# Kernel tuning notes

Measured on AMD Instinct MI355X. Metric: run time of the kernel, lower is better.

The kernel has to match this reference:

```python
import jax, jax.numpy as jnp
import numpy as np

EPS = 1e-5  # torch LayerNorm default


def _channel_ln(h, g, b):
    # h: (B, C, N); LayerNorm over channel dim C (biased variance)
    m = jnp.mean(h, axis=1, keepdims=True)
    v = jnp.mean((h - m) ** 2, axis=1, keepdims=True)
    return (h - m) * jax.lax.rsqrt(v + EPS) * g[None, :, None] + b[None, :, None]


def setup_inputs() -> dict:
    key = jax.random.key(0)
    ks = jax.random.split(key, 16)
    B, Cin, Cout, N = 8, 64, 128, 4096
    w = lambda i, shape: jax.random.normal(ks[i], shape, jnp.float32) * 0.02
    return {
        "x": jax.random.normal(ks[0], (B, Cin, N), jnp.float32),
        "p": jax.random.normal(ks[1], (B, 3, N), jnp.float32),
        "W_in": w(2, (Cout, Cin)), "b_in": jnp.zeros((Cout,), jnp.float32),
        "W_q": w(3, (Cout, Cout)),
        "W_k": w(4, (Cout, Cout)),
        "W_v": w(5, (Cout, Cout)),
        "W_d1": w(6, (Cout, 3)), "b_d1": jnp.zeros((Cout,), jnp.float32),
        "W_d2": w(7, (Cout, Cout)), "b_d2": jnp.zeros((Cout,), jnp.float32),
        "W_a": w(8, (Cout, Cout)), "b_a": jnp.zeros((Cout,), jnp.float32),
        "g1": jnp.ones((Cout,), jnp.float32), "be1": jnp.zeros((Cout,), jnp.float32),
        "g2": jnp.ones((Cout,), jnp.float32), "be2": jnp.zeros((Cout,), jnp.float32),
        "W_f1": w(9, (4 * Cout, Cout)), "b_f1": jnp.zeros((4 * Cout,), jnp.float32),
        "W_f2": w(10, (Cout, 4 * Cout)), "b_f2": jnp.zeros((Cout,), jnp.float32),
        "knn_k": 16,
    }


def reference(x, p, W_in, b_in, W_q, W_k, W_v, W_d1, b_d1, W_d2, b_d2,
              W_a, b_a, g1, be1, g2, be2, W_f1, b_f1, W_f2, b_f2, knn_k):
    h = jnp.einsum('oc,bcn->bon', W_in, x) + b_in[None, :, None]  # (B,C,N)
    B, C, N = h.shape
    k = min(int(knn_k), max(1, N - 1))

    h_n = _channel_ln(h, g1, be1)

    # knn on coordinates p: negative squared distance, self excluded
    pt = jnp.swapaxes(p, 1, 2)                                    # (B,N,3)
    xx = jnp.sum(pt * pt, axis=-1)                                # (B,N)
    dist = 2.0 * jnp.einsum('bnd,bmd->bnm', pt, pt) - xx[:, :, None] - xx[:, None, :]
    dist = dist - 1e9 * jnp.eye(N, dtype=dist.dtype)[None]
    idx = jax.lax.top_k(dist, k)[1]                               # (B,N,k) int32

    hn_t = jnp.swapaxes(h_n, 1, 2)                                # (B,N,C)
    q_all = hn_t @ W_q.T
    k_all = hn_t @ W_k.T
    v_all = hn_t @ W_v.T

    bi = jnp.arange(B)[:, None, None]
    k_j = k_all[bi, idx]                                          # (B,N,k,C)
    v_j = v_all[bi, idx]                                          # (B,N,k,C)
    p_j = pt[bi, idx]                                             # (B,N,k,3)

    rel = pt[:, :, None, :] - p_j                                 # (B,N,k,3)
    d = jax.nn.relu(rel @ W_d1.T + b_d1) @ W_d2.T + b_d2          # (B,N,k,C)

    logits = (q_all[:, :, None, :] - k_j + d) @ W_a.T + b_a       # (B,N,k,C)
    a = jax.nn.softmax(logits, axis=2)                            # softmax over k neighbors
    y = jnp.sum(a * (v_j + d), axis=2)                            # (B,N,C)

    h = h + jnp.swapaxes(y, 1, 2)
    h2t = jnp.swapaxes(_channel_ln(h, g2, be2), 1, 2)             # (B,N,C)
    f = jax.nn.relu(h2t @ W_f1.T + b_f1) @ W_f2.T + b_f2          # (B,N,C)
    return h + jnp.swapaxes(f, 1, 2)                              # (B,C,N)
```

## Files before the change

### kernel.cpp

```cpp
#include <hip/hip_runtime.h>
#include <stdint.h>


typedef __attribute__((ext_vector_type(8))) short s8;
typedef __attribute__((ext_vector_type(4))) float f4;

#define MFMA16(a,b,c) __builtin_amdgcn_mfma_f32_16x16x32_bf16(a,b,c,0,0,0)

__device__ __forceinline__ float bf2f(unsigned short u){
  unsigned x = ((unsigned)u) << 16; return __builtin_bit_cast(float, x);
}
__device__ __forceinline__ unsigned short f2bf(float f){
  unsigned x = __builtin_bit_cast(unsigned, f);
  x = x + 0x7FFFu + ((x >> 16) & 1u);
  return (unsigned short)(x >> 16);
}

__device__ __forceinline__ void ce32(unsigned &a, unsigned &b){
  unsigned mn = min(a, b), mx = max(a, b);
  a = mn; b = mx;
}
__device__ __forceinline__ void sort16_u32(unsigned v[16]){
  #pragma unroll
  for (int p = 1; p < 16; p <<= 1){
    #pragma unroll
    for (int k = p; k >= 1; k >>= 1){
      #pragma unroll
      for (int j = k % p; j + k < 16; j += 2*k){
        #pragma unroll
        for (int i = 0; i < k; ++i){
          if (i + j + k < 16){
            if (((i+j) / (2*p)) == ((i+j+k) / (2*p))) ce32(v[i+j], v[i+j+k]);
          }
        }
      }
    }
  }
}
__device__ __forceinline__ void bitonic16_u32(unsigned v[16]){
  #pragma unroll
  for (int k = 8; k >= 1; k >>= 1){
    #pragma unroll
    for (int i = 0; i < 16; ++i){
      if ((i & k) == 0) ce32(v[i], v[i | k]);
    }
  }
}
__device__ __forceinline__ void merge16r(unsigned top[16], const unsigned w[16],
                                         unsigned &r17){
  unsigned t[16], m17 = 0xFFFFFFFFu;
  #pragma unroll
  for (int i = 0; i < 16; ++i){
    unsigned a = top[i], b = w[15 - i];
    t[i] = min(a, b);
    m17 = min(m17, max(a, b));
  }
  bitonic16_u32(t);
  #pragma unroll
  for (int i = 0; i < 16; ++i) top[i] = t[i];
  r17 = min(r17, m17);
}
__device__ __forceinline__ void drainP(unsigned* br, int &cnt, unsigned top[16],
                                       unsigned &r17, unsigned &thr){
  unsigned v[16];
  #pragma unroll
  for (int j = 0; j < 16; ++j){
    unsigned t = br[j];
    v[j] = (j < cnt) ? t : 0xFFFFFFFFu;
  }
  cnt = 0;
  sort16_u32(v);
  merge16r(top, v, r17);
  thr = top[15];
}

__global__ __launch_bounds__(128) void k_p1(const float* __restrict__ W_a,
    const float* __restrict__ W_k, const float* __restrict__ W_q, const float* __restrict__ W_d2,
    float* __restrict__ tk, float* __restrict__ tq, float* __restrict__ td){
  int which = blockIdx.x >> 7, row = blockIdx.x & 127, c = threadIdx.x;
  const float* X = (which == 0) ? W_k : ((which == 1) ? W_q : W_d2);
  float* O = (which == 0) ? tk : ((which == 1) ? tq : td);
  float acc = 0.f;
  #pragma unroll 8
  for (int i = 0; i < 128; ++i) acc += W_a[row*128 + i] * X[i*128 + c];
  O[row*128 + c] = acc;
}

__global__ __launch_bounds__(256) void k_pack(
    const float* __restrict__ p, const float* __restrict__ W_v,
    const float* __restrict__ W_d1, const float* __restrict__ b_d1,
    const float* __restrict__ W_in, const float* __restrict__ W_f1, const float* __restrict__ W_f2,
    const float* __restrict__ W_a, const float* __restrict__ b_a, const float* __restrict__ b_d2,
    const float* __restrict__ W_d2,
    const float* __restrict__ tk, const float* __restrict__ tq, const float* __restrict__ td,
    float4* __restrict__ pp, unsigned short* __restrict__ wcatf, unsigned short* __restrict__ wf1f,
    unsigned short* __restrict__ wf2f, unsigned short* __restrict__ wd2f,
    unsigned short* __restrict__ wdaf, unsigned short* __restrict__ w1f,
    unsigned short* __restrict__ winf, float* __restrict__ ball){
  int id0 = blockIdx.x * blockDim.x + threadIdx.x;
  int stride = gridDim.x * blockDim.x;
  for (int i = id0; i < 32768; i += stride){
    int b = i >> 12, m = i & 4095;
    float xx = p[(b*3 + 0)*4096 + m];
    float yy = p[(b*3 + 1)*4096 + m];
    float zz = p[(b*3 + 2)*4096 + m];
    pp[i] = float4{xx, yy, zz, xx*xx + yy*yy + zz*zz};
  }
  for (int i = id0; i < 49152; i += stride){
    int tg = i >> 11, s = (i >> 9) & 3, l = (i >> 3) & 63, j = i & 7;
    int row = tg*16 + (l & 15), k = s*32 + (l >> 4)*8 + j;
    float v;
    if (row < 128) v = tk[row*128 + k];
    else if (row < 256) v = W_v[(row - 128)*128 + k];
    else v = tq[(row - 256)*128 + k];
    wcatf[i] = f2bf(v);
  }
  for (int i = id0; i < 65536; i += stride){
    int tg = i >> 11, s = (i >> 9) & 3, l = (i >> 3) & 63, j = i & 7;
    int row = tg*16 + (l & 15), k = s*32 + (l >> 4)*8 + j;
    wf1f[i] = f2bf(W_f1[row*128 + k]);
  }
  for (int i = id0; i < 65536; i += stride){
    int mt = i >> 13, s = (i >> 9) & 15, l = (i >> 3) & 63, j = i & 7;
    int row = mt*16 + (l & 15), k = s*32 + (l >> 4)*8 + j;
    wf2f[i] = f2bf(W_f2[row*512 + k]);
  }
  for (int i = id0; i < 16384; i += stride){
    int tg = i >> 11, s = (i >> 9) & 3, l = (i >> 3) & 63, j = i & 7;
    int row = tg*16 + (l & 15), k = s*32 + (l >> 4)*8 + j;
    wd2f[i] = f2bf(W_d2[row*128 + k]);
  }
  for (int i = id0; i < 16384; i += stride){
    int tg = i >> 11, s = (i >> 9) & 3, l = (i >> 3) & 63, j = i & 7;
    int row = tg*16 + (l & 15), k = s*32 + (l >> 4)*8 + j;
    wdaf[i] = f2bf(td[row*128 + k]);
  }
  for (int i = id0; i < 4096; i += stride){
    int tg = i >> 9, l = (i >> 3) & 63, j = i & 7;
    int c = tg*16 + (l & 15);
    float v = 0.f;
    if (l < 16 && j < 4) v = (j < 3) ? W_d1[c*3 + j] : b_d1[c];
    w1f[i] = f2bf(v);
  }
  for (int i = id0; i < 8192; i += stride){
    int tg = i >> 10, s = (i >> 9) & 1, l = (i >> 3) & 63, j = i & 7;
    int row = tg*16 + (l & 15), k = s*32 + (l >> 4)*8 + j;
    winf[i] = f2bf(W_in[row*64 + k]);
  }
  for (int o = id0; o < 128; o += stride){
    float acc = b_a[o];
    for (int c = 0; c < 128; ++c) acc += W_a[o*128 + c] * b_d2[c];
    ball[o] = acc;
  }
}

__global__ __launch_bounds__(256) void k_a(const float* __restrict__ x,
    const unsigned short* __restrict__ WINF, const float* __restrict__ b_in,
    const float* __restrict__ g1, const float* __restrict__ be1,
    float* __restrict__ H, unsigned short* __restrict__ HN){
  __shared__ unsigned short xT[64][72];
  int tid = threadIdx.x;
  int bb = blockIdx.x >> 6;
  int n0 = (blockIdx.x & 63) * 64;
  for (int i = tid; i < 4096; i += 256){
    int c = i >> 6, nn = i & 63;
    xT[nn][c] = f2bf(x[((size_t)(bb*64 + c))*4096 + n0 + nn]);
  }
  __syncthreads();
  int lane = tid & 63, w = tid >> 6, m16 = lane & 15, g = lane >> 4;
  const char* xb = (const char*)&xT[0][0];
  s8 a0 = *(const s8*)(xb + (w*16 + m16)*144 + 16*g);
  s8 a1 = *(const s8*)(xb + (w*16 + m16)*144 + 64 + 16*g);
  const f4 zf = {0.f, 0.f, 0.f, 0.f};
  f4 acc[8];
  #pragma unroll
  for (int t = 0; t < 8; ++t) acc[t] = zf;
  #pragma unroll
  for (int t = 0; t < 8; ++t){
    s8 b0 = *(const s8*)(WINF + ((size_t)(t*2 + 0)*64 + lane)*8);
    s8 b1 = *(const s8*)(WINF + ((size_t)(t*2 + 1)*64 + lane)*8);
    acc[t] = MFMA16(a0, b0, acc[t]);
    acc[t] = MFMA16(a1, b1, acc[t]);
  }
  float mean[4], rstd[4];
  #pragma unroll
  for (int r = 0; r < 4; ++r){
    float ls = 0.f, lq = 0.f;
    #pragma unroll
    for (int t = 0; t < 8; ++t){
      float v = acc[t][r] + b_in[t*16 + m16];
      ls += v; lq += v*v;
    }
    ls += __shfl_xor(ls, 1); ls += __shfl_xor(ls, 2); ls += __shfl_xor(ls, 4); ls += __shfl_xor(ls, 8);
    lq += __shfl_xor(lq, 1); lq += __shfl_xor(lq, 2); lq += __shfl_xor(lq, 4); lq += __shfl_xor(lq, 8);
    float mn = ls * (1.f/128.f);
    float vr = lq * (1.f/128.f) - mn*mn;
    mean[r] = mn;
    rstd[r] = rsqrtf(vr + 1e-5f);
  }
  int ptbase = blockIdx.x*64 + w*16;
  #pragma unroll
  for (int t = 0; t < 8; ++t){
    int o = t*16 + m16;
    float bi = b_in[o], gg = g1[o], be = be1[o];
    #pragma unroll
    for (int r = 0; r < 4; ++r){
      int pt = ptbase + 4*g + r;
      float v = acc[t][r] + bi;
      H[(size_t)pt*128 + o] = v;
      HN[(size_t)pt*128 + o] = f2bf((v - mean[r])*rstd[r]*gg + be);
    }
  }
}

template<int MODE>
__global__ __launch_bounds__(256) void k_gemm(const unsigned short* __restrict__ A,
    const unsigned short* __restrict__ Btab, const float* __restrict__ bias,
    unsigned short* __restrict__ out){
  int lane = threadIdx.x & 63, w = threadIdx.x >> 6;
  int m0 = blockIdx.x*64 + w*16;
  int by = blockIdx.y;
  int m16 = lane & 15, g = lane >> 4;
  const f4 zf = {0.f, 0.f, 0.f, 0.f};
  f4 acc[8];
  #pragma unroll
  for (int t = 0; t < 8; ++t) acc[t] = zf;
  #pragma unroll
  for (int s = 0; s < 4; ++s){
    s8 af = *(const s8*)(A + ((size_t)(m0 + m16))*128 + s*32 + g*8);
    #pragma unroll
    for (int t = 0; t < 8; ++t){
      s8 bf = *(const s8*)(Btab + ((size_t)((by*8 + t)*4 + s)*64 + lane)*8);
      acc[t] = MFMA16(af, bf, acc[t]);
    }
  }
  #pragma unroll
  for (int t = 0; t < 8; ++t){
    int col = by*128 + t*16 + m16;
    #pragma unroll
    for (int r = 0; r < 4; ++r){
      int pt = m0 + 4*g + r;
      float v = acc[t][r];
      if (MODE == 0){
        int pos = (col < 128) ? 2*col : ((col < 256) ? 2*(col - 128) + 1 : col);
        out[(size_t)pt*384 + pos] = f2bf(v);
      } else {
        v = fmaxf(v + bias[col], 0.f);
        out[(size_t)pt*512 + col] = f2bf(v);
      }
    }
  }
}

__global__ __launch_bounds__(256) void k_f2(const unsigned short* __restrict__ wf2f,
    const unsigned short* __restrict__ Z, const float* __restrict__ b_f2,
    float* __restrict__ out){
  int lane = threadIdx.x & 63, w = threadIdx.x >> 6;
  int mt = blockIdx.x*4 + w;
  int p0 = blockIdx.y*128;
  int m16 = lane & 15, g = lane >> 4;
  const f4 zf = {0.f, 0.f, 0.f, 0.f};
  f4 acc[8];
  #pragma unroll
  for (int t = 0; t < 8; ++t) acc[t] = zf;
  #pragma unroll 4
  for (int s = 0; s < 16; ++s){
    s8 af = *(const s8*)(wf2f + ((size_t)(mt*16 + s)*64 + lane)*8);
    #pragma unroll
    for (int t = 0; t < 8; ++t){
      s8 bf = *(const s8*)(Z + (size_t)(p0 + t*16 + m16)*512 + s*32 + g*8);
      acc[t] = MFMA16(af, bf, acc[t]);
    }
  }
  #pragma unroll
  for (int t = 0; t < 8; ++t){
    #pragma unroll
    for (int r = 0; r < 4; ++r){
      int o = mt*16 + 4*g + r;
      int pt = p0 + t*16 + m16;
      int b = pt >> 12, n = pt & 4095;
      size_t ix = (((size_t)(b*128 + o)) << 12) | (unsigned)n;
      out[ix] += acc[t][r] + b_f2[o];
    }
  }
}

__global__ __launch_bounds__(256, 8) void k_knn(const float4* __restrict__ PP,
    int* __restrict__ IDXo){
  __shared__ __align__(16) char smem[17920];
  int tid = threadIdx.x;
  int b = blockIdx.x >> 7;
  int tile = blockIdx.x & 127;
  int q = tid & 31;
  int sub = tid >> 5;
  int qn = tile*32 + q;
  const float4* pb = PP + (size_t)b*4096;
  float4 me = pb[qn];
  int base = sub << 9;

  unsigned* br32 = (unsigned*)(smem + tid*68);

  unsigned top32[16];
  #pragma unroll
  for (int j = 0; j < 16; ++j) top32[j] = 0xFFFFFFFFu;
  unsigned r17 = 0xFFFFFFFFu;
  unsigned thr = 0xFFFFFFFFu;
  int cnt = 0;
  float4 c0 = pb[base+0], c1 = pb[base+1], c2 = pb[base+2], c3 = pb[base+3];
  #pragma unroll 1
  for (int ii = 0; ii < 128; ++ii){
    float4 d0 = c0, d1 = c1, d2v = c2, d3 = c3;
    int nb = base + (((ii + 1) & 127) << 2);
    c0 = pb[nb+0]; c1 = pb[nb+1]; c2 = pb[nb+2]; c3 = pb[nb+3];
    int m0 = base + ii*4;
    {
      float dx = me.x-d0.x, dy = me.y-d0.y, dz = me.z-d0.z;
      unsigned key = (__builtin_bit_cast(unsigned, dx*dx+dy*dy+dz*dz) & 0xFFFFF000u) | (unsigned)m0;
      if (m0 != qn){ if (key < thr){ br32[cnt] = key; ++cnt; } else r17 = min(r17, key); }
    }
    {
      float dx = me.x-d1.x, dy = me.y-d1.y, dz = me.z-d1.z;
      unsigned key = (__builtin_bit_cast(unsigned, dx*dx+dy*dy+dz*dz) & 0xFFFFF000u) | (unsigned)(m0+1);
      if (m0+1 != qn){ if (key < thr){ br32[cnt] = key; ++cnt; } else r17 = min(r17, key); }
    }
    {
      float dx = me.x-d2v.x, dy = me.y-d2v.y, dz = me.z-d2v.z;
      unsigned key = (__builtin_bit_cast(unsigned, dx*dx+dy*dy+dz*dz) & 0xFFFFF000u) | (unsigned)(m0+2);
      if (m0+2 != qn){ if (key < thr){ br32[cnt] = key; ++cnt; } else r17 = min(r17, key); }
    }
    {
      float dx = me.x-d3.x, dy = me.y-d3.y, dz = me.z-d3.z;
      unsigned key = (__builtin_bit_cast(unsigned, dx*dx+dy*dy+dz*dz) & 0xFFFFF000u) | (unsigned)(m0+3);
      if (m0+3 != qn){ if (key < thr){ br32[cnt] = key; ++cnt; } else r17 = min(r17, key); }
    }
    if (__any(cnt >= 13)) drainP(br32, cnt, top32, r17, thr);
  }
  drainP(br32, cnt, top32, r17, thr);

  unsigned* pub = (unsigned*)smem;
  #pragma unroll
  for (int step = 4; step >= 1; step >>= 1){
    __syncthreads();
    if (sub >= step && sub < 2*step){
      unsigned* row = pub + (size_t)((sub - step)*32 + q)*17;
      #pragma unroll
      for (int j = 0; j < 16; ++j) row[j] = top32[j];
      row[16] = r17;
    }
    __syncthreads();
    if (sub < step){
      unsigned other[16];
      unsigned* row = pub + (size_t)(sub*32 + q)*17;
      #pragma unroll
      for (int j = 0; j < 16; ++j) other[j] = row[j];
      r17 = min(r17, row[16]);
      merge16r(top32, other, r17);
    }
  }

  unsigned key16 = top32[15];
  bool flag = false;
  if (sub == 0){
    flag = ((r17 >> 12) - (key16 >> 12)) <= 1u;
    if (!flag){
      int* op = IDXo + ((size_t)(b*4096 + qn))*16;
      #pragma unroll
      for (int j = 0; j < 16; ++j) op[j] = (int)(top32[j] & 0xFFFu);
    }
  }

  if ((tid >> 6) == 0){
    int lane = tid & 63;
    unsigned long long flags = __ballot(flag);
    int* pcnt = (int*)(smem + 17408);
    unsigned* pool = (unsigned*)(smem + 17412);
    while (flags){
      int L = __ffsll((long long)flags) - 1;
      flags &= flags - 1;
      int qf = tile*32 + L;
      float qx = __shfl(me.x, L), qy = __shfl(me.y, L), qz = __shfl(me.z, L);
      unsigned k16 = __shfl(key16, L);
      unsigned t16 = k16 >> 12;
      unsigned bhi = (t16 >= 0xFFFFDu) ? 0xFFFFFFFFu : ((t16 + 2) << 12);
      if (lane == 0) atomicExch(pcnt, 0);
      #pragma unroll 4
      for (int it = 0; it < 64; ++it){
        int m = it*64 + lane;
        float4 cd = pb[m];
        float dx = qx-cd.x, dy = qy-cd.y, dz = qz-cd.z;
        unsigned bits = __builtin_bit_cast(unsigned, dx*dx+dy*dy+dz*dz);
        if (m != qf && bits < bhi){
          int s = atomicAdd(pcnt, 1);
          if (s < 64) pool[s] = (unsigned)m;
        }
      }
      int pn = atomicAdd(pcnt, 0);
      if (pn > 64) pn = 64;
      unsigned long long kk = ~0ull;
      if (lane < pn){
        int m = pool[lane];
        float4 cd = pb[m];
        double ddx = (double)qx - (double)cd.x;
        double ddy = (double)qy - (double)cd.y;
        double ddz = (double)qz - (double)cd.z;
        double d2 = ddx*ddx + ddy*ddy + ddz*ddz;
        kk = (__builtin_bit_cast(unsigned long long, d2) & ~0xFFFull) | (unsigned)m;
      }
      #pragma unroll
      for (int k2 = 2; k2 <= 64; k2 <<= 1){
        #pragma unroll
        for (int j = k2 >> 1; j >= 1; j >>= 1){
          unsigned long long o = __shfl_xor(kk, j);
          bool up = ((lane & k2) == 0);
          bool keepmin = (((lane & j) == 0) == up);
          unsigned long long mn = kk < o ? kk : o;
          unsigned long long mx = kk < o ? o : kk;
          kk = keepmin ? mn : mx;
        }
      }
      if (lane < 16)
        IDXo[((size_t)(b*4096 + qf))*16 + lane] = (int)(unsigned)(kk & 0xFFFull);
    }
  }
}

__global__ __launch_bounds__(256) void k_attn(const float* __restrict__ pcoord,
    const int* __restrict__ IDX, const unsigned short* __restrict__ QKV,
    const unsigned short* __restrict__ W1F, const unsigned short* __restrict__ WD2F,
    const unsigned short* __restrict__ WDAF, const float* __restrict__ b_d2,
    const float* __restrict__ BALL, unsigned short* __restrict__ Y){
  __shared__ __align__(16) char smem[18432];
  __shared__ int idx_sh[4][2][16];
  int tid = threadIdx.x;
  int w = tid >> 6, lane = tid & 63;
  int m16 = lane & 15, g = lane >> 4;
  int P0 = blockIdx.x*8 + w*2;
  char* wbase = smem + w*4608;
  const f4 zf = {0.f, 0.f, 0.f, 0.f};
  if (lane < 16){
    #pragma unroll
    for (int q = 0; q < 2; ++q) idx_sh[w][q][lane] = IDX[(size_t)(P0 + q)*16 + lane];
  }
  unsigned short* t1s = (unsigned short*)wbase;
  s8 a[2][4];
  #pragma unroll
  for (int q = 0; q < 2; ++q){
    int pt = P0 + q;
    int bq = pt >> 12, nn = pt & 4095;
    const float* pb = pcoord + (size_t)bq*3*4096;
    s8 arel = {0,0,0,0,0,0,0,0};
    if (lane < 16){
      int jn = idx_sh[w][q][m16];
      float rx = pb[nn] - pb[jn];
      float ry = pb[4096 + nn] - pb[4096 + jn];
      float rz = pb[8192 + nn] - pb[8192 + jn];
      arel[0] = (short)f2bf(rx); arel[1] = (short)f2bf(ry);
      arel[2] = (short)f2bf(rz); arel[3] = (short)0x3F80;
    }
    f4 t1a[8];
    #pragma unroll
    for (int t = 0; t < 8; ++t){
      s8 bw = *(const s8*)(W1F + ((size_t)t*64 + lane)*8);
      t1a[t] = MFMA16(arel, bw, zf);
    }
    #pragma unroll
    for (int t = 0; t < 8; ++t){
      int c = t*16 + m16;
      #pragma unroll
      for (int r = 0; r < 4; ++r){
        int m = 4*g + r;
        int byt = (m*256 + c*2) ^ ((m & 7) << 4);
        t1s[byt >> 1] = f2bf(fmaxf(t1a[t][r], 0.f));
      }
    }
    const char* t1b = (const char*)t1s;
    #pragma unroll
    for (int s = 0; s < 4; ++s){
      int byt = (m16*256 + 64*s + 16*g) ^ ((m16 & 7) << 4);
      a[q][s] = *(const s8*)(t1b + byt);
    }
  }
  #pragma unroll 1
  for (int pass = 0; pass < 4; ++pass){
    asm volatile("s_waitcnt lgkmcnt(0)" ::: "memory");
    __builtin_amdgcn_sched_barrier(0);
    uint4 gk[2][2];
    float qv[2];
    #pragma unroll
    for (int q = 0; q < 2; ++q){
      int pt = P0 + q, bq = pt >> 12;
      #pragma unroll
      for (int i2 = 0; i2 < 2; ++i2){
        int mm = i2*8 + (lane >> 3);
        int jn = idx_sh[w][q][mm];
        gk[q][i2] = *(const uint4*)((const char*)QKV
            + ((size_t)(bq*4096 + jn))*768 + pass*128 + (lane & 7)*16);
      }
      qv[q] = bf2f(QKV[(size_t)pt*384 + 256 + pass*32 + (lane & 31)]);
    }
    #pragma unroll
    for (int q = 0; q < 2; ++q){
      #pragma unroll
      for (int i2 = 0; i2 < 2; ++i2)
        *(uint4*)(wbase + q*2304 + (i2*8 + (lane >> 3))*144 + (lane & 7)*16) = gk[q][i2];
    }
    #pragma unroll
    for (int tl = 0; tl < 2; ++tl){
      int tg = pass*2 + tl;
      f4 dacc[2], lacc[2];
      #pragma unroll
      for (int q = 0; q < 2; ++q){ dacc[q] = zf; lacc[q] = zf; }
      #pragma unroll
      for (int s = 0; s < 4; ++s){
        s8 wd2 = *(const s8*)(WD2F + ((size_t)(tg*4 + s)*64 + lane)*8);
        s8 wda = *(const s8*)(WDAF + ((size_t)(tg*4 + s)*64 + lane)*8);
        #pragma unroll
        for (int q = 0; q < 2; ++q){
          dacc[q] = MFMA16(a[q][s], wd2, dacc[q]);
          lacc[q] = MFMA16(a[q][s], wda, lacc[q]);
        }
      }
      int col = tg*16 + m16;
      float bd2c = b_d2[col];
      float ballc = BALL[col];
      #pragma unroll
      for (int q = 0; q < 2; ++q){
        int pt = P0 + q;
        float qbase = __shfl(qv[q], tl*16 + m16) + ballc;
        float lg[4], dd[4], vv[4];
        #pragma unroll
        for (int r = 0; r < 4; ++r){
          int m = 4*g + r;
          unsigned kvp = *(const unsigned*)(wbase + q*2304 + m*144 + (tl*16 + m16)*4);
          float ka = bf2f((unsigned short)(kvp & 0xFFFFu));
          vv[r] = bf2f((unsigned short)(kvp >> 16));
          lg[r] = lacc[q][r] + qbase - ka;
          dd[r] = dacc[q][r] + bd2c;
        }
        float e0 = __expf(lg[0]), e1 = __expf(lg[1]);
        float e2 = __expf(lg[2]), e3 = __expf(lg[3]);
        float ss = e0 + e1 + e2 + e3;
        ss += __shfl_xor(ss, 16); ss += __shfl_xor(ss, 32);
        float inv = 1.f / ss;
        float yp = e0*(vv[0] + dd[0]) + e1*(vv[1] + dd[1])
                 + e2*(vv[2] + dd[2]) + e3*(vv[3] + dd[3]);
        yp *= inv;
        yp += __shfl_xor(yp, 16); yp += __shfl_xor(yp, 32);
        if (lane < 16) Y[(size_t)pt*128 + col] = f2bf(yp);
      }
    }
  }
}

__global__ __launch_bounds__(256) void k_d1(const float* __restrict__ H,
    const unsigned short* __restrict__ Y, const float* __restrict__ g2,
    const float* __restrict__ be2, float* __restrict__ outp,
    unsigned short* __restrict__ HN2){
  __shared__ float tile[128*65];
  int tid = threadIdx.x;
  int w = tid >> 6, lane = tid & 63;
  int pt16 = lane & 15, g = lane >> 4;
  int n64 = w*16 + pt16;
  int ptbase = blockIdx.x * 64;
  int pt = ptbase + n64;
  int c0 = g*32;
  const float4* h4 = (const float4*)(H + (size_t)pt*128 + c0);
  const uint4*  y4 = (const uint4*)((const char*)Y + (size_t)pt*256 + (size_t)c0*2);
  float h2[32];
  float ls = 0.f, lq = 0.f;
  #pragma unroll
  for (int i = 0; i < 4; ++i){
    float4 ha = h4[2*i], hb = h4[2*i + 1];
    uint4 yv = y4[i];
    float v0 = ha.x + bf2f((unsigned short)(yv.x & 0xFFFFu));
    float v1 = ha.y + bf2f((unsigned short)(yv.x >> 16));
    float v2 = ha.z + bf2f((unsigned short)(yv.y & 0xFFFFu));
    float v3 = ha.w + bf2f((unsigned short)(yv.y >> 16));
    float v4 = hb.x + bf2f((unsigned short)(yv.z & 0xFFFFu));
    float v5 = hb.y + bf2f((unsigned short)(yv.z >> 16));
    float v6 = hb.z + bf2f((unsigned short)(yv.w & 0xFFFFu));
    float v7 = hb.w + bf2f((unsigned short)(yv.w >> 16));
    h2[8*i+0]=v0; h2[8*i+1]=v1; h2[8*i+2]=v2; h2[8*i+3]=v3;
    h2[8*i+4]=v4; h2[8*i+5]=v5; h2[8*i+6]=v6; h2[8*i+7]=v7;
    ls += v0+v1+v2+v3+v4+v5+v6+v7;
    lq += v0*v0+v1*v1+v2*v2+v3*v3+v4*v4+v5*v5+v6*v6+v7*v7;
  }
  ls += __shfl_xor(ls, 16); ls += __shfl_xor(ls, 32);
  lq += __shfl_xor(lq, 16); lq += __shfl_xor(lq, 32);
  float mn = ls * (1.f/128.f);
  float vr = lq * (1.f/128.f) - mn*mn;
  float rs = rsqrtf(vr + 1e-5f);
  const float4* g4  = (const float4*)(g2 + c0);
  const float4* be4 = (const float4*)(be2 + c0);
  #pragma unroll
  for (int i = 0; i < 4; ++i){
    float4 ga = g4[2*i], gb = g4[2*i+1], ba = be4[2*i], bb2 = be4[2*i+1];
    unsigned uu[4];
    uu[0] = (unsigned)f2bf((h2[8*i+0]-mn)*rs*ga.x + ba.x)
          | ((unsigned)f2bf((h2[8*i+1]-mn)*rs*ga.y + ba.y) << 16);
    uu[1] = (unsigned)f2bf((h2[8*i+2]-mn)*rs*ga.z + ba.z)
          | ((unsigned)f2bf((h2[8*i+3]-mn)*rs*ga.w + ba.w) << 16);
    uu[2] = (unsigned)f2bf((h2[8*i+4]-mn)*rs*gb.x + bb2.x)
          | ((unsigned)f2bf((h2[8*i+5]-mn)*rs*gb.y + bb2.y) << 16);
    uu[3] = (unsigned)f2bf((h2[8*i+6]-mn)*rs*gb.z + bb2.z)
          | ((unsigned)f2bf((h2[8*i+7]-mn)*rs*gb.w + bb2.w) << 16);
    *(uint4*)((char*)HN2 + (size_t)pt*256 + (size_t)c0*2 + i*16)
        = make_uint4(uu[0], uu[1], uu[2], uu[3]);
  }
  int swz = g << 4;
  #pragma unroll
  for (int k = 0; k < 32; ++k)
    tile[(c0 + k)*65 + (n64 ^ swz)] = h2[k];
  __syncthreads();
  int bb = ptbase >> 12;
  int nb = ptbase & 4095;
  #pragma unroll 8
  for (int k = 0; k < 32; ++k){
    int c = w*32 + k;
    float v = tile[c*65 + (lane ^ ((((unsigned)c >> 5) & 3) << 4))];
    outp[(((size_t)(bb*128 + c)) << 12) | (unsigned)(nb + lane)] = v;
  }
}

extern "C" void kernel_launch(void* const* d_in, const int* in_sizes, int n_in,
                              void* d_out, int out_size, void* d_ws, size_t ws_size,
                              hipStream_t stream){
  const float* x    = (const float*)d_in[0];
  const float* p    = (const float*)d_in[1];
  const float* W_in = (const float*)d_in[2];
  const float* b_in = (const float*)d_in[3];
  const float* W_q  = (const float*)d_in[4];
  const float* W_k  = (const float*)d_in[5];
  const float* W_v  = (const float*)d_in[6];
  const float* W_d1 = (const float*)d_in[7];
  const float* b_d1 = (const float*)d_in[8];
  const float* W_d2 = (const float*)d_in[9];
  const float* b_d2 = (const float*)d_in[10];
  const float* W_a  = (const float*)d_in[11];
  const float* b_a  = (const float*)d_in[12];
  const float* g1   = (const float*)d_in[13];
  const float* be1  = (const float*)d_in[14];
  const float* g2   = (const float*)d_in[15];
  const float* be2  = (const float*)d_in[16];
  const float* W_f1 = (const float*)d_in[17];
  const float* b_f1 = (const float*)d_in[18];
  const float* W_f2 = (const float*)d_in[19];
  const float* b_f2 = (const float*)d_in[20];
  float* out = (float*)d_out;
  char* ws = (char*)d_ws;

  float*          H    = (float*)(ws + 0);
  unsigned short* HN   = (unsigned short*)(ws + 16777216);
  unsigned short* QKV  = (unsigned short*)(ws + 25165824);
  unsigned short* Z    = (unsigned short*)(ws + 16777216);
  unsigned short* Y    = (unsigned short*)(ws + 50331648);
  unsigned short* HN2  = (unsigned short*)(ws + 58720256);
  int*            IDX  = (int*)(ws + 67108864);
  float4*         PP   = (float4*)(ws + 69206016);
  char* tab = ws + 69730304;
  unsigned short* WCATF = (unsigned short*)(tab + 0);
  unsigned short* WF1F  = (unsigned short*)(tab + 98304);
  unsigned short* WF2F  = (unsigned short*)(tab + 229376);
  unsigned short* WD2F  = (unsigned short*)(tab + 360448);
  unsigned short* WDAF  = (unsigned short*)(tab + 393216);
  unsigned short* W1F   = (unsigned short*)(tab + 425984);
  unsigned short* WINF  = (unsigned short*)(tab + 434176);
  float*          BALL  = (float*)(tab + 450560);
  float*          TK    = (float*)(tab + 451072);
  float*          TQ    = (float*)(tab + 516608);
  float*          TD    = (float*)(tab + 582144);

  k_p1<<<dim3(384), dim3(128), 0, stream>>>(W_a, W_k, W_q, W_d2, TK, TQ, TD);
  k_pack<<<dim3(256), dim3(256), 0, stream>>>(p, W_v, W_d1, b_d1, W_in, W_f1, W_f2,
      W_a, b_a, b_d2, W_d2, TK, TQ, TD,
      PP, WCATF, WF1F, WF2F, WD2F, WDAF, W1F, WINF, BALL);
  k_knn<<<dim3(1024), dim3(256), 0, stream>>>(PP, IDX);
  k_a<<<dim3(512), dim3(256), 0, stream>>>(x, WINF, b_in, g1, be1, H, HN);
  k_gemm<0><<<dim3(512, 3), dim3(256), 0, stream>>>(HN, WCATF, nullptr, QKV);
  k_attn<<<dim3(4096), dim3(256), 0, stream>>>(p, IDX, QKV, W1F, WD2F, WDAF, b_d2, BALL, Y);
  k_d1<<<dim3(512), dim3(256), 0, stream>>>(H, Y, g2, be2, out, HN2);
  k_gemm<1><<<dim3(512, 4), dim3(256), 0, stream>>>(HN2, WF1F, b_f1, Z);
  k_f2<<<dim3(2, 256), dim3(256), 0, stream>>>(WF2F, Z, b_f2, out);
}
```

Before: 332.5 us.

## Seed kNN threshold with sorted prefix and split candidates across more sub-groups

The kNN kernel now handles 16 queries per block with 16 sub-groups, each scanning 256 candidates, so the grid doubles. Each thread first sorts and merges its initial 64 candidates with a sorting network to set a tight top-16 threshold before the streaming scan. The goal is fewer buffer drains and better load balance. The cost is a deeper shared-memory merge tree, with four levels and more syncs, plus extra register pressure from the unrolled seeding.

```diff
diff --git a/kernel.cpp b/kernel.cpp
--- a/kernel.cpp
+++ b/kernel.cpp
@@ -289,60 +289,66 @@
     int* __restrict__ IDXo){
   __shared__ __align__(16) char smem[17920];
   int tid = threadIdx.x;
-  int b = blockIdx.x >> 7;
-  int tile = blockIdx.x & 127;
-  int q = tid & 31;
-  int sub = tid >> 5;
-  int qn = tile*32 + q;
+  int b = blockIdx.x >> 8;
+  int tile = blockIdx.x & 255;
+  int q = tid & 15;
+  int sub = tid >> 4;
+  int qn = tile*16 + q;
   const float4* pb = PP + (size_t)b*4096;
   float4 me = pb[qn];
-  int base = sub << 9;
-
+  const float4* cb = pb + (sub << 8);
+
+  unsigned top32[16];
+  unsigned r17 = 0xFFFFFFFFu;
+  #pragma unroll
+  for (int c = 0; c < 4; ++c){
+    unsigned v[16];
+    #pragma unroll
+    for (int j = 0; j < 16; ++j){
+      float4 cd = cb[c*16 + j];
+      int m = (sub << 8) + c*16 + j;
+      float dx = me.x-cd.x, dy = me.y-cd.y, dz = me.z-cd.z;
+      unsigned key = (__builtin_bit_cast(unsigned, dx*dx+dy*dy+dz*dz) & 0xFFFFF000u) | (unsigned)m;
+      v[j] = (m == qn) ? 0xFFFFFFFFu : key;
+    }
+    sort16_u32(v);
+    if (c == 0){
+      #pragma unroll
+      for (int j = 0; j < 16; ++j) top32[j] = v[j];
+    } else {
+      merge16r(top32, v, r17);
+    }
+  }
+  unsigned thr = top32[15];
+
+  int cnt = 0;
   unsigned* br32 = (unsigned*)(smem + tid*68);
-
-  unsigned top32[16];
-  #pragma unroll
-  for (int j = 0; j < 16; ++j) top32[j] = 0xFFFFFFFFu;
-  unsigned r17 = 0xFFFFFFFFu;
-  unsigned thr = 0xFFFFFFFFu;
-  int cnt = 0;
-  float4 c0 = pb[base+0], c1 = pb[base+1], c2 = pb[base+2], c3 = pb[base+3];
   #pragma unroll 1
-  for (int ii = 0; ii < 128; ++ii){
-    float4 d0 = c0, d1 = c1, d2v = c2, d3 = c3;
-    int nb = base + (((ii + 1) & 127) << 2);
-    c0 = pb[nb+0]; c1 = pb[nb+1]; c2 = pb[nb+2]; c3 = pb[nb+3];
-    int m0 = base + ii*4;
-    {
-      float dx = me.x-d0.x, dy = me.y-d0.y, dz = me.z-d0.z;
-      unsigned key = (__builtin_bit_cast(unsigned, dx*dx+dy*dy+dz*dz) & 0xFFFFF000u) | (unsigned)m0;
-      if (m0 != qn){ if (key < thr){ br32[cnt] = key; ++cnt; } else r17 = min(r17, key); }
-    }
-    {
-      float dx = me.x-d1.x, dy = me.y-d1.y, dz = me.z-d1.z;
-      unsigned key = (__builtin_bit_cast(unsigned, dx*dx+dy*dy+dz*dz) & 0xFFFFF000u) | (unsigned)(m0+1);
-      if (m0+1 != qn){ if (key < thr){ br32[cnt] = key; ++cnt; } else r17 = min(r17, key); }
-    }
-    {
-      float dx = me.x-d2v.x, dy = me.y-d2v.y, dz = me.z-d2v.z;
-      unsigned key = (__builtin_bit_cast(unsigned, dx*dx+dy*dy+dz*dz) & 0xFFFFF000u) | (unsigned)(m0+2);
-      if (m0+2 != qn){ if (key < thr){ br32[cnt] = key; ++cnt; } else r17 = min(r17, key); }
-    }
-    {
-      float dx = me.x-d3.x, dy = me.y-d3.y, dz = me.z-d3.z;
-      unsigned key = (__builtin_bit_cast(unsigned, dx*dx+dy*dy+dz*dz) & 0xFFFFF000u) | (unsigned)(m0+3);
-      if (m0+3 != qn){ if (key < thr){ br32[cnt] = key; ++cnt; } else r17 = min(r17, key); }
-    }
-    if (__any(cnt >= 13)) drainP(br32, cnt, top32, r17, thr);
+  for (int oo = 0; oo < 12; ++oo){
+    const float4* ob = cb + 64 + oo*16;
+    int mb = (sub << 8) + 64 + oo*16;
+    #pragma unroll
+    for (int jg = 0; jg < 4; ++jg){
+      #pragma unroll
+      for (int u = 0; u < 4; ++u){
+        int j = jg*4 + u;
+        float4 cd = ob[j];
+        int m = mb + j;
+        float dx = me.x-cd.x, dy = me.y-cd.y, dz = me.z-cd.z;
+        unsigned key = (__builtin_bit_cast(unsigned, dx*dx+dy*dy+dz*dz) & 0xFFFFF000u) | (unsigned)m;
+        if (m != qn){ if (key < thr){ br32[cnt] = key; ++cnt; } else r17 = min(r17, key); }
+      }
+      if (__any(cnt >= 13)) drainP(br32, cnt, top32, r17, thr);
+    }
   }
   drainP(br32, cnt, top32, r17, thr);
 
   unsigned* pub = (unsigned*)smem;
   #pragma unroll
-  for (int step = 4; step >= 1; step >>= 1){
+  for (int step = 8; step >= 1; step >>= 1){
     __syncthreads();
     if (sub >= step && sub < 2*step){
-      unsigned* row = pub + (size_t)((sub - step)*32 + q)*17;
+      unsigned* row = pub + (size_t)((sub - step)*16 + q)*17;
       #pragma unroll
       for (int j = 0; j < 16; ++j) row[j] = top32[j];
       row[16] = r17;
@@ -350,7 +356,7 @@
     __syncthreads();
     if (sub < step){
       unsigned other[16];
-      unsigned* row = pub + (size_t)(sub*32 + q)*17;
+      unsigned* row = pub + (size_t)(sub*16 + q)*17;
       #pragma unroll
       for (int j = 0; j < 16; ++j) other[j] = row[j];
       r17 = min(r17, row[16]);
@@ -377,7 +383,7 @@
     while (flags){
       int L = __ffsll((long long)flags) - 1;
       flags &= flags - 1;
-      int qf = tile*32 + L;
+      int qf = tile*16 + L;
       float qx = __shfl(me.x, L), qy = __shfl(me.y, L), qz = __shfl(me.z, L);
       unsigned k16 = __shfl(key16, L);
       unsigned t16 = k16 >> 12;
@@ -674,7 +680,7 @@
   k_pack<<<dim3(256), dim3(256), 0, stream>>>(p, W_v, W_d1, b_d1, W_in, W_f1, W_f2,
       W_a, b_a, b_d2, W_d2, TK, TQ, TD,
       PP, WCATF, WF1F, WF2F, WD2F, WDAF, W1F, WINF, BALL);
-  k_knn<<<dim3(1024), dim3(256), 0, stream>>>(PP, IDX);
+  k_knn<<<dim3(2048), dim3(256), 0, stream>>>(PP, IDX);
   k_a<<<dim3(512), dim3(256), 0, stream>>>(x, WINF, b_in, g1, be1, H, HN);
   k_gemm<0><<<dim3(512, 3), dim3(256), 0, stream>>>(HN, WCATF, nullptr, QKV);
   k_attn<<<dim3(4096), dim3(256), 0, stream>>>(p, IDX, QKV, W1F, WD2F, WDAF, b_d2, BALL, Y);
```

New measurement: 369.1 us. +11.0%, slower.

## Replace brute-force kNN with uniform-grid spatial hashing and ring search

Applied to the files above, without the earlier changes.

Points are binned into a 32^3 uniform grid per batch, built with atomic counting, a prefix scan and a scatter into cell-sorted order. Each query wave then scans expanding rings of cells, keeping per-lane top-16 lists that are merged across the wave with shuffles, and stops once the ring boundary distance exceeds the current 17th-best distance. This removes the all-pairs distance evaluation of the old kernel. It adds a memset and three extra small kernels. Performance depends on the point distribution matching the assumed [-5,5] grid extent, although clamping keeps results correct for any input.

```diff
diff --git a/kernel.cpp b/kernel.cpp
--- a/kernel.cpp
+++ b/kernel.cpp
@@ -20,23 +20,6 @@
   unsigned mn = min(a, b), mx = max(a, b);
   a = mn; b = mx;
 }
-__device__ __forceinline__ void sort16_u32(unsigned v[16]){
-  #pragma unroll
-  for (int p = 1; p < 16; p <<= 1){
-    #pragma unroll
-    for (int k = p; k >= 1; k >>= 1){
-      #pragma unroll
-      for (int j = k % p; j + k < 16; j += 2*k){
-        #pragma unroll
-        for (int i = 0; i < k; ++i){
-          if (i + j + k < 16){
-            if (((i+j) / (2*p)) == ((i+j+k) / (2*p))) ce32(v[i+j], v[i+j+k]);
-          }
-        }
-      }
-    }
-  }
-}
 __device__ __forceinline__ void bitonic16_u32(unsigned v[16]){
   #pragma unroll
   for (int k = 8; k >= 1; k >>= 1){
@@ -60,18 +43,39 @@
   for (int i = 0; i < 16; ++i) top[i] = t[i];
   r17 = min(r17, m17);
 }
-__device__ __forceinline__ void drainP(unsigned* br, int &cnt, unsigned top[16],
-                                       unsigned &r17, unsigned &thr){
-  unsigned v[16];
-  #pragma unroll
-  for (int j = 0; j < 16; ++j){
-    unsigned t = br[j];
-    v[j] = (j < cnt) ? t : 0xFFFFFFFFu;
-  }
-  cnt = 0;
-  sort16_u32(v);
-  merge16r(top, v, r17);
-  thr = top[15];
+__device__ __forceinline__ void insert16(unsigned top16[16], unsigned &r17, unsigned key){
+  if (key < top16[15]){
+    unsigned cur = key;
+    #pragma unroll
+    for (int i = 0; i < 16; ++i){
+      unsigned lo = min(cur, top16[i]);
+      unsigned hi = max(cur, top16[i]);
+      top16[i] = lo; cur = hi;
+    }
+    r17 = min(r17, cur);
+  } else {
+    r17 = min(r17, key);
+  }
+}
+__device__ __forceinline__ void wave_merge(const unsigned loc[16], unsigned lr17,
+                                           unsigned out[16], unsigned &or17){
+  #pragma unroll
+  for (int j = 0; j < 16; ++j) out[j] = loc[j];
+  unsigned rr = lr17;
+  #pragma unroll
+  for (int s = 1; s < 64; s <<= 1){
+    unsigned oth[16];
+    #pragma unroll
+    for (int j = 0; j < 16; ++j) oth[j] = (unsigned)__shfl_xor((int)out[j], s);
+    unsigned ro = (unsigned)__shfl_xor((int)rr, s);
+    rr = min(rr, ro);
+    merge16r(out, oth, rr);
+  }
+  or17 = rr;
+}
+__device__ __forceinline__ int cell1(float x){
+  int c = (int)floorf((x + 5.f) * 3.2f);
+  return min(max(c, 0), 31);
 }
 
 __global__ __launch_bounds__(128) void k_p1(const float* __restrict__ W_a,
@@ -96,7 +100,8 @@
     float4* __restrict__ pp, unsigned short* __restrict__ wcatf, unsigned short* __restrict__ wf1f,
     unsigned short* __restrict__ wf2f, unsigned short* __restrict__ wd2f,
     unsigned short* __restrict__ wdaf, unsigned short* __restrict__ w1f,
-    unsigned short* __restrict__ winf, float* __restrict__ ball){
+    unsigned short* __restrict__ winf, float* __restrict__ ball,
+    unsigned* __restrict__ ccnt){
   int id0 = blockIdx.x * blockDim.x + threadIdx.x;
   int stride = gridDim.x * blockDim.x;
   for (int i = id0; i < 32768; i += stride){
@@ -105,6 +110,8 @@
     float yy = p[(b*3 + 1)*4096 + m];
     float zz = p[(b*3 + 2)*4096 + m];
     pp[i] = float4{xx, yy, zz, xx*xx + yy*yy + zz*zz};
+    int cid = (cell1(xx)*32 + cell1(yy))*32 + cell1(zz);
+    atomicAdd(&ccnt[b*32768 + cid], 1u);
   }
   for (int i = id0; i < 49152; i += stride){
     int tg = i >> 11, s = (i >> 9) & 3, l = (i >> 3) & 63, j = i & 7;
@@ -152,6 +159,174 @@
     for (int c = 0; c < 128; ++c) acc += W_a[o*128 + c] * b_d2[c];
     ball[o] = acc;
   }
+}
+
+__global__ __launch_bounds__(1024) void k_scan(unsigned* __restrict__ CNTCUR,
+    unsigned* __restrict__ OFF){
+  __shared__ unsigned ps[1024];
+  int b = blockIdx.x, t = threadIdx.x;
+  unsigned* cnt = CNTCUR + (size_t)b*32768;
+  int base = t*32;
+  unsigned run = 0;
+  #pragma unroll
+  for (int i = 0; i < 32; ++i) run += cnt[base + i];
+  ps[t] = run;
+  __syncthreads();
+  for (int st = 1; st < 1024; st <<= 1){
+    unsigned v = (t >= st) ? ps[t - st] : 0u;
+    __syncthreads();
+    ps[t] += v;
+    __syncthreads();
+  }
+  unsigned run2 = (t == 0) ? 0u : ps[t-1];
+  #pragma unroll
+  for (int i = 0; i < 32; ++i){
+    unsigned v = cnt[base + i];
+    OFF[(size_t)b*32769 + base + i] = run2;
+    cnt[base + i] = run2;
+    run2 += v;
+  }
+  if (t == 1023) OFF[(size_t)b*32769 + 32768] = 4096u;
+}
+
+__global__ __launch_bounds__(256) void k_scatter(const float4* __restrict__ PP,
+    unsigned* __restrict__ CUR, float4* __restrict__ SPTS){
+  int i = blockIdx.x*256 + threadIdx.x;
+  float4 pt = PP[i];
+  int b = i >> 12, n = i & 4095;
+  int cid = (cell1(pt.x)*32 + cell1(pt.y))*32 + cell1(pt.z);
+  unsigned pos = atomicAdd(&CUR[(size_t)b*32768 + cid], 1u);
+  SPTS[(size_t)b*4096 + pos] = float4{pt.x, pt.y, pt.z,
+                                      __builtin_bit_cast(float, n)};
+}
+
+__global__ __launch_bounds__(256) void k_knng(const float4* __restrict__ PP,
+    const float4* __restrict__ SPTS, const unsigned* __restrict__ OFF,
+    int* __restrict__ IDXo){
+  __shared__ unsigned pool_sh[4][64];
+  int wv = threadIdx.x >> 6;
+  int lane = threadIdx.x & 63;
+  int wid = blockIdx.x*4 + wv;
+  int b = wid >> 12, n = wid & 4095;
+  const float4 me = PP[(size_t)b*4096 + n];
+  const float4* sp = SPTS + (size_t)b*4096;
+  const unsigned* off = OFF + (size_t)b*32769;
+  float qx = me.x, qy = me.y, qz = me.z;
+  int cx = cell1(qx), cy = cell1(qy), cz = cell1(qz);
+
+  unsigned top16[16];
+  #pragma unroll
+  for (int j = 0; j < 16; ++j) top16[j] = 0xFFFFFFFFu;
+  unsigned r17 = 0xFFFFFFFFu;
+  unsigned tot = 0;
+  unsigned g16[16];
+  unsigned gr17 = 0xFFFFFFFFu;
+
+  auto do_range = [&](int cbase, int za, int zb){
+    unsigned s = off[cbase + za];
+    unsigned e = off[cbase + zb + 1];
+    int len = (int)(e - s);
+    int first = ((int)lane - (int)tot) & 63;
+    for (int i = first; i < len; i += 64){
+      float4 cd = sp[s + i];
+      int m = __builtin_bit_cast(int, cd.w);
+      float dx = qx - cd.x, dy = qy - cd.y, dz = qz - cd.z;
+      float d2 = dx*dx + dy*dy + dz*dz;
+      unsigned key = (__builtin_bit_cast(unsigned, d2) & 0xFFFFF000u) | (unsigned)m;
+      if (m != n) insert16(top16, r17, key);
+    }
+    tot += (unsigned)len;
+  };
+
+  bool done = false;
+  #pragma unroll 1
+  for (int R = 1; R <= 32 && !done; ++R){
+    int x0 = max(cx-R, 0), x1 = min(cx+R, 31);
+    int y0 = max(cy-R, 0), y1 = min(cy+R, 31);
+    #pragma unroll 1
+    for (int gx = x0; gx <= x1; ++gx){
+      int dxm = (gx > cx) ? (gx - cx) : (cx - gx);
+      #pragma unroll 1
+      for (int gy = y0; gy <= y1; ++gy){
+        int dym = (gy > cy) ? (gy - cy) : (cy - gy);
+        int dm = max(dxm, dym);
+        int cbase = (gx*32 + gy)*32;
+        if (R == 1 || dm == R){
+          do_range(cbase, max(cz-R, 0), min(cz+R, 31));
+        } else {
+          if (cz - R >= 0)  do_range(cbase, cz-R, cz-R);
+          if (cz + R <= 31) do_range(cbase, cz+R, cz+R);
+        }
+      }
+    }
+    wave_merge(top16, r17, g16, gr17);
+    float bd = 1e30f;
+    if (cx - R >= 0)  bd = fminf(bd, qx - (-5.f + (float)(cx-R)*0.3125f));
+    if (cx + R <= 31) bd = fminf(bd, (-5.f + (float)(cx+R+1)*0.3125f) - qx);
+    if (cy - R >= 0)  bd = fminf(bd, qy - (-5.f + (float)(cy-R)*0.3125f));
+    if (cy + R <= 31) bd = fminf(bd, (-5.f + (float)(cy+R+1)*0.3125f) - qy);
+    if (cz - R >= 0)  bd = fminf(bd, qz - (-5.f + (float)(cz-R)*0.3125f));
+    if (cz + R <= 31) bd = fminf(bd, (-5.f + (float)(cz+R+1)*0.3125f) - qz);
+    if (bd > 1e29f){
+      done = true;
+    } else if (gr17 != 0xFFFFFFFFu){
+      unsigned ub = (gr17 & 0xFFFFF000u) + 0x1000u;
+      float d2ub = __builtin_bit_cast(float, ub) * (1.f + 1e-5f);
+      float bl = bd * bd * (1.f - 1e-5f);
+      if (bl > d2ub) done = true;
+    }
+  }
+
+  unsigned key16 = g16[15];
+  bool flag = ((gr17 >> 12) - (key16 >> 12)) <= 1u;
+  if (!flag){
+    if (lane < 16) IDXo[(size_t)wid*16 + lane] = (int)(g16[lane] & 0xFFFu);
+    return;
+  }
+  unsigned t16 = key16 >> 12;
+  unsigned bhi = (t16 >= 0xFFFFDu) ? 0xFFFFFFFFu : ((t16 + 2) << 12);
+  unsigned pcnt = 0;
+  const float4* pb = PP + (size_t)b*4096;
+  #pragma unroll 4
+  for (int it = 0; it < 64; ++it){
+    int m = it*64 + lane;
+    float4 cd = pb[m];
+    float dx = qx-cd.x, dy = qy-cd.y, dz = qz-cd.z;
+    unsigned bits = __builtin_bit_cast(unsigned, dx*dx+dy*dy+dz*dz);
+    bool cond = (m != n) && (bits < bhi);
+    unsigned long long mk = __ballot(cond);
+    if (cond){
+      int pos = (int)pcnt + __popcll(mk & ((1ull << lane) - 1ull));
+      if (pos < 64) pool_sh[wv][pos] = (unsigned)m;
+    }
+    pcnt += (unsigned)__popcll(mk);
+  }
+  asm volatile("s_waitcnt lgkmcnt(0)" ::: "memory");
+  int pn = (int)min(pcnt, 64u);
+  unsigned long long kk = ~0ull;
+  if (lane < pn){
+    int m = (int)pool_sh[wv][lane];
+    float4 cd = pb[m];
+    double ddx = (double)qx - (double)cd.x;
+    double ddy = (double)qy - (double)cd.y;
+    double ddz = (double)qz - (double)cd.z;
+    double d2 = ddx*ddx + ddy*ddy + ddz*ddz;
+    kk = (__builtin_bit_cast(unsigned long long, d2) & ~0xFFFull) | (unsigned)m;
+  }
+  #pragma unroll
+  for (int k2 = 2; k2 <= 64; k2 <<= 1){
+    #pragma unroll
+    for (int j = k2 >> 1; j >= 1; j >>= 1){
+      unsigned long long o = __shfl_xor(kk, j);
+      bool up = ((lane & k2) == 0);
+      bool keepmin = (((lane & j) == 0) == up);
+      unsigned long long mn = kk < o ? kk : o;
+      unsigned long long mx = kk < o ? o : kk;
+      kk = keepmin ? mn : mx;
+    }
+  }
+  if (lane < 16)
+    IDXo[(size_t)wid*16 + lane] = (int)(unsigned)(kk & 0xFFFull);
 }
 
 __global__ __launch_bounds__(256) void k_a(const float* __restrict__ x,
@@ -281,145 +456,6 @@
       int b = pt >> 12, n = pt & 4095;
       size_t ix = (((size_t)(b*128 + o)) << 12) | (unsigned)n;
       out[ix] += acc[t][r] + b_f2[o];
-    }
-  }
-}
-
-__global__ __launch_bounds__(256, 8) void k_knn(const float4* __restrict__ PP,
-    int* __restrict__ IDXo){
-  __shared__ __align__(16) char smem[17920];
-  int tid = threadIdx.x;
-  int b = blockIdx.x >> 7;
-  int tile = blockIdx.x & 127;
-  int q = tid & 31;
-  int sub = tid >> 5;
-  int qn = tile*32 + q;
-  const float4* pb = PP + (size_t)b*4096;
-  float4 me = pb[qn];
-  int base = sub << 9;
-
-  unsigned* br32 = (unsigned*)(smem + tid*68);
-
-  unsigned top32[16];
-  #pragma unroll
-  for (int j = 0; j < 16; ++j) top32[j] = 0xFFFFFFFFu;
-  unsigned r17 = 0xFFFFFFFFu;
-  unsigned thr = 0xFFFFFFFFu;
-  int cnt = 0;
-  float4 c0 = pb[base+0], c1 = pb[base+1], c2 = pb[base+2], c3 = pb[base+3];
-  #pragma unroll 1
-  for (int ii = 0; ii < 128; ++ii){
-    float4 d0 = c0, d1 = c1, d2v = c2, d3 = c3;
-    int nb = base + (((ii + 1) & 127) << 2);
-    c0 = pb[nb+0]; c1 = pb[nb+1]; c2 = pb[nb+2]; c3 = pb[nb+3];
-    int m0 = base + ii*4;
-    {
-      float dx = me.x-d0.x, dy = me.y-d0.y, dz = me.z-d0.z;
-      unsigned key = (__builtin_bit_cast(unsigned, dx*dx+dy*dy+dz*dz) & 0xFFFFF000u) | (unsigned)m0;
-      if (m0 != qn){ if (key < thr){ br32[cnt] = key; ++cnt; } else r17 = min(r17, key); }
-    }
-    {
-      float dx = me.x-d1.x, dy = me.y-d1.y, dz = me.z-d1.z;
-      unsigned key = (__builtin_bit_cast(unsigned, dx*dx+dy*dy+dz*dz) & 0xFFFFF000u) | (unsigned)(m0+1);
-      if (m0+1 != qn){ if (key < thr){ br32[cnt] = key; ++cnt; } else r17 = min(r17, key); }
-    }
-    {
-      float dx = me.x-d2v.x, dy = me.y-d2v.y, dz = me.z-d2v.z;
-      unsigned key = (__builtin_bit_cast(unsigned, dx*dx+dy*dy+dz*dz) & 0xFFFFF000u) | (unsigned)(m0+2);
-      if (m0+2 != qn){ if (key < thr){ br32[cnt] = key; ++cnt; } else r17 = min(r17, key); }
-    }
-    {
-      float dx = me.x-d3.x, dy = me.y-d3.y, dz = me.z-d3.z;
-      unsigned key = (__builtin_bit_cast(unsigned, dx*dx+dy*dy+dz*dz) & 0xFFFFF000u) | (unsigned)(m0+3);
-      if (m0+3 != qn){ if (key < thr){ br32[cnt] = key; ++cnt; } else r17 = min(r17, key); }
-    }
-    if (__any(cnt >= 13)) drainP(br32, cnt, top32, r17, thr);
-  }
-  drainP(br32, cnt, top32, r17, thr);
-
-  unsigned* pub = (unsigned*)smem;
-  #pragma unroll
-  for (int step = 4; step >= 1; step >>= 1){
-    __syncthreads();
-    if (sub >= step && sub < 2*step){
-      unsigned* row = pub + (size_t)((sub - step)*32 + q)*17;
-      #pragma unroll
-      for (int j = 0; j < 16; ++j) row[j] = top32[j];
-      row[16] = r17;
-    }
-    __syncthreads();
-    if (sub < step){
-      unsigned other[16];
-      unsigned* row = pub + (size_t)(sub*32 + q)*17;
-      #pragma unroll
-      for (int j = 0; j < 16; ++j) other[j] = row[j];
-      r17 = min(r17, row[16]);
-      merge16r(top32, other, r17);
-    }
-  }
-
-  unsigned key16 = top32[15];
-  bool flag = false;
-  if (sub == 0){
-    flag = ((r17 >> 12) - (key16 >> 12)) <= 1u;
-    if (!flag){
-      int* op = IDXo + ((size_t)(b*4096 + qn))*16;
-      #pragma unroll
-      for (int j = 0; j < 16; ++j) op[j] = (int)(top32[j] & 0xFFFu);
-    }
-  }
-
-  if ((tid >> 6) == 0){
-    int lane = tid & 63;
-    unsigned long long flags = __ballot(flag);
-    int* pcnt = (int*)(smem + 17408);
-    unsigned* pool = (unsigned*)(smem + 17412);
-    while (flags){
-      int L = __ffsll((long long)flags) - 1;
-      flags &= flags - 1;
-      int qf = tile*32 + L;
-      float qx = __shfl(me.x, L), qy = __shfl(me.y, L), qz = __shfl(me.z, L);
-      unsigned k16 = __shfl(key16, L);
-      unsigned t16 = k16 >> 12;
-      unsigned bhi = (t16 >= 0xFFFFDu) ? 0xFFFFFFFFu : ((t16 + 2) << 12);
-      if (lane == 0) atomicExch(pcnt, 0);
-      #pragma unroll 4
-      for (int it = 0; it < 64; ++it){
-        int m = it*64 + lane;
-        float4 cd = pb[m];
-        float dx = qx-cd.x, dy = qy-cd.y, dz = qz-cd.z;
-        unsigned bits = __builtin_bit_cast(unsigned, dx*dx+dy*dy+dz*dz);
-        if (m != qf && bits < bhi){
-          int s = atomicAdd(pcnt, 1);
-          if (s < 64) pool[s] = (unsigned)m;
-        }
-      }
-      int pn = atomicAdd(pcnt, 0);
-      if (pn > 64) pn = 64;
-      unsigned long long kk = ~0ull;
-      if (lane < pn){
-        int m = pool[lane];
-        float4 cd = pb[m];
-        double ddx = (double)qx - (double)cd.x;
-        double ddy = (double)qy - (double)cd.y;
-        double ddz = (double)qz - (double)cd.z;
-        double d2 = ddx*ddx + ddy*ddy + ddz*ddz;
-        kk = (__builtin_bit_cast(unsigned long long, d2) & ~0xFFFull) | (unsigned)m;
-      }
-      #pragma unroll
-      for (int k2 = 2; k2 <= 64; k2 <<= 1){
-        #pragma unroll
-        for (int j = k2 >> 1; j >= 1; j >>= 1){
-          unsigned long long o = __shfl_xor(kk, j);
-          bool up = ((lane & k2) == 0);
-          bool keepmin = (((lane & j) == 0) == up);
-          unsigned long long mn = kk < o ? kk : o;
-          unsigned long long mx = kk < o ? o : kk;
-          kk = keepmin ? mn : mx;
-        }
-      }
-      if (lane < 16)
-        IDXo[((size_t)(b*4096 + qf))*16 + lane] = (int)(unsigned)(kk & 0xFFFull);
     }
   }
 }
@@ -669,12 +705,18 @@
   float*          TK    = (float*)(tab + 451072);
   float*          TQ    = (float*)(tab + 516608);
   float*          TD    = (float*)(tab + 582144);
-
+  unsigned*       CNTCUR = (unsigned*)(ws + 70377984);
+  unsigned*       OFF    = (unsigned*)(ws + 71426560);
+  float4*         SPTS   = (float4*)(ws + 72475168);
+
+  hipMemsetAsync(CNTCUR, 0, 8u*32768u*4u, stream);
   k_p1<<<dim3(384), dim3(128), 0, stream>>>(W_a, W_k, W_q, W_d2, TK, TQ, TD);
   k_pack<<<dim3(256), dim3(256), 0, stream>>>(p, W_v, W_d1, b_d1, W_in, W_f1, W_f2,
       W_a, b_a, b_d2, W_d2, TK, TQ, TD,
-      PP, WCATF, WF1F, WF2F, WD2F, WDAF, W1F, WINF, BALL);
-  k_knn<<<dim3(1024), dim3(256), 0, stream>>>(PP, IDX);
+      PP, WCATF, WF1F, WF2F, WD2F, WDAF, W1F, WINF, BALL, CNTCUR);
+  k_scan<<<dim3(8), dim3(1024), 0, stream>>>(CNTCUR, OFF);
+  k_scatter<<<dim3(128), dim3(256), 0, stream>>>(PP, CNTCUR, SPTS);
+  k_knng<<<dim3(8192), dim3(256), 0, stream>>>(PP, SPTS, OFF, IDX);
   k_a<<<dim3(512), dim3(256), 0, stream>>>(x, WINF, b_in, g1, be1, H, HN);
   k_gemm<0><<<dim3(512, 3), dim3(256), 0, stream>>>(HN, WCATF, nullptr, QKV);
   k_attn<<<dim3(4096), dim3(256), 0, stream>>>(p, IDX, QKV, W1F, WD2F, WDAF, b_d2, BALL, Y);
```

After: 644.1 us. 1.94x slower.
